# Kernel optimization log

Hardware: AMD Instinct MI355X
Metric: run time of the kernel (lower is better)

The kernel has to match this reference:

```python
import jax, jax.numpy as jnp
import numpy as np

NUM_SLOTS = 7
DIM = 4096
NUM_HEADS = 8
HEAD_DIM = DIM // NUM_HEADS
LN_EPS = 1e-5


def setup_inputs() -> dict:
    key = jax.random.key(0)
    ks = jax.random.split(key, 9)
    B, N = 8, 2048
    x = jax.random.normal(ks[0], (B, N, DIM), dtype=jnp.float32)
    slots = 1e-4 * jax.random.normal(ks[1], (NUM_SLOTS, DIM), dtype=jnp.float32)
    ln_g = jnp.ones((DIM,), jnp.float32)
    ln_b = jnp.zeros((DIM,), jnp.float32)
    # nn.MultiheadAttention packed in-projection: rows [Wq; Wk; Wv], each (DIM, DIM)
    s = 1.0 / np.sqrt(DIM)
    in_proj_w = jax.random.uniform(ks[2], (3 * DIM, DIM), jnp.float32, -s, s)
    in_proj_b = jnp.zeros((3 * DIM,), jnp.float32)
    out_proj_w = jax.random.uniform(ks[3], (DIM, DIM), jnp.float32, -s, s)
    out_proj_b = jnp.zeros((DIM,), jnp.float32)
    alpha = 0.1 * jax.random.normal(ks[4], (1,), jnp.float32)  # nonzero so gate path is active
    return {"x": x, "slots": slots, "ln_g": ln_g, "ln_b": ln_b,
            "in_proj_w": in_proj_w, "in_proj_b": in_proj_b,
            "out_proj_w": out_proj_w, "out_proj_b": out_proj_b, "alpha": alpha}


def _cmrm(x, slots, ln_g, ln_b, in_proj_w, in_proj_b, out_proj_w, out_proj_b, alpha):
    x32 = x.astype(jnp.float32)
    # pre LayerNorm
    mu = jnp.mean(x32, axis=-1, keepdims=True)
    var = jnp.mean(jnp.square(x32 - mu), axis=-1, keepdims=True)
    xn = (x32 - mu) * jax.lax.rsqrt(var + LN_EPS) * ln_g + ln_b  # (B,N,D)
    slots_c = jnp.clip(slots, -10.0, 10.0)  # (Q,D), Q=7
    Wq, Wk, Wv = jnp.split(in_proj_w, 3, axis=0)
    bq, bk, bv = jnp.split(in_proj_b, 3, axis=0)
    q = slots_c @ Wq.T + bq                      # (Q,D), identical for all batches
    k = xn @ Wk.T + bk                           # (B,N,D)
    v = xn @ Wv.T + bv                           # (B,N,D)
    B, N, _ = x.shape
    qh = q.reshape(NUM_SLOTS, NUM_HEADS, HEAD_DIM)          # (Q,H,hd)
    kh = k.reshape(B, N, NUM_HEADS, HEAD_DIM)
    vh = v.reshape(B, N, NUM_HEADS, HEAD_DIM)
    scale = 1.0 / np.sqrt(HEAD_DIM)
    scores = jnp.einsum('qhd,bnhd->bhqn', qh * scale, kh)   # (B,H,Q,N)
    attn = jax.nn.softmax(scores, axis=-1)
    ctx = jnp.einsum('bhqn,bnhd->bqhd', attn, vh).reshape(B, NUM_SLOTS, DIM)
    slots_out = ctx @ out_proj_w.T + out_proj_b             # (B,Q,D)
    slots_res = slots_c[None] + slots_out                   # residual, ungated slots
    gate = jnp.tanh(alpha)                                  # (1,)
    g = jnp.mean(gate * slots_res, axis=1, keepdims=True)   # (B,1,D)
    x_refined = (x32 + g).astype(x.dtype)
    attn_weights = jnp.mean(attn, axis=1)                   # torch avg over heads -> (B,Q,N)
    return x_refined, attn_weights


def reference(x, slots, ln_g, ln_b, in_proj_w, in_proj_b, out_proj_w, out_proj_b, alpha):
    return _cmrm(x, slots, ln_g, ln_b, in_proj_w, in_proj_b, out_proj_w, out_proj_b, alpha)
```

## Files before the change

### kernel.cpp

```cpp
#include <hip/hip_runtime.h>

typedef __attribute__((ext_vector_type(4))) float f32x4;
typedef __attribute__((ext_vector_type(8))) short short8x;
typedef __attribute__((ext_vector_type(4))) unsigned short u16x4;

#define DIM   4096
#define NB    8
#define NN    2048
#define NROWS (NB*NN)
#define NQ    7
#define NHQ   56
#define SCALE 0.04419417382415922f

#define OFF_MU     0L
#define OFF_RSTD   16384L
#define OFF_Q7     32768L
#define OFF_A      61440L
#define OFF_D0     61504L
#define OFF_S1     61568L
#define OFF_SUMEXP 61632L
#define OFF_CTXM   62528L
#define OFF_GFIN   95296L
#define OFF_YM     128064L
#define OFF_UGBF   390208L
#define OFF_SCT    521280L
#define OFF_BIG    1438784L
#define OFF_PART   (OFF_BIG)
#define OFF_XBF    10000000L

__device__ __forceinline__ unsigned short f2bf(float f) {
  union { float f; unsigned int u; } v; v.f = f;
  return (unsigned short)((v.u + 0x7FFFu + ((v.u >> 16) & 1u)) >> 16);
}
__device__ __forceinline__ unsigned short f2bfr(float f) {
  union { float f; unsigned int u; } v; v.f = f;
  return (unsigned short)((v.u + 0x8000u) >> 16);
}
__device__ __forceinline__ float bf2f(unsigned short u) {
  return __uint_as_float((unsigned)u << 16);
}
__device__ __forceinline__ f32x4 ntl4(const float* p) {
  return __builtin_nontemporal_load((const f32x4*)p);
}
__device__ __forceinline__ void nts4(float* p, f32x4 v) {
  __builtin_nontemporal_store(v, (f32x4*)p);
}
__device__ __forceinline__ float waveSum(float v) {
  #pragma unroll
  for (int m = 1; m < 64; m <<= 1) v += __shfl_xor(v, m);
  return v;
}

__global__ __launch_bounds__(256) void k_pre(const float* __restrict__ ipw,
    const float* __restrict__ ipb, const float* __restrict__ slots,
    float* __restrict__ q7, float* __restrict__ ws) {
  const int bid = blockIdx.x, tid = threadIdx.x;
  const int w = tid >> 6, l = tid & 63;
  if (bid == 0) {
    if (tid < 448) (ws + OFF_SUMEXP)[tid] = 0.f;
    else if (tid < 512) (ws + OFF_S1)[tid - 448] = 0.f;
  } else if (bid <= 8) {
    unsigned* u32 = (unsigned*)(ws + OFF_UGBF);
    const long r = 56 + bid - 1;
    #pragma unroll
    for (int j = 0; j < 8; j++) u32[r*2048 + (long)tid*8 + j] = 0u;
  } else if (bid == 9) {
    if (tid < 64) (ws + OFF_A)[tid] = 0.f;
    else if (tid < 128) (ws + OFF_D0)[tid - 64] = 0.f;
  }
  const int d = bid * 4 + w;
  const float* wr = ipw + (long)d * DIM;
  float acc[7] = {0,0,0,0,0,0,0};
  for (int e4 = l; e4 < 1024; e4 += 64) {
    f32x4 wv = ntl4(wr + e4*4);
    #pragma unroll
    for (int s = 0; s < 7; s++) {
      float4 sv = ((const float4*)(slots + (long)s*DIM))[e4];
      sv.x = fminf(fmaxf(sv.x, -10.f), 10.f); sv.y = fminf(fmaxf(sv.y, -10.f), 10.f);
      sv.z = fminf(fmaxf(sv.z, -10.f), 10.f); sv.w = fminf(fmaxf(sv.w, -10.f), 10.f);
      acc[s] += wv.x*sv.x + wv.y*sv.y + wv.z*sv.z + wv.w*sv.w;
    }
  }
  #pragma unroll
  for (int s = 0; s < 7; s++) acc[s] = waveSum(acc[s]);
  if (l == 0) {
    float bq = ipb[d];
    #pragma unroll
    for (int s = 0; s < 7; s++) q7[(long)s*DIM + d] = acc[s] + bq;
  }
}

__global__ __launch_bounds__(256) void k_uproj(const float* __restrict__ ipw,
    const float* __restrict__ ipb, const float* __restrict__ q7,
    float* __restrict__ upart, float* __restrict__ D0arr) {
  __shared__ float qs[7][32];
  const int bid = blockIdx.x, tid = threadIdx.x;
  const int bx = bid & 3, h = (bid >> 2) & 7, c = bid >> 5;
  if (tid < 224) {
    int s = tid >> 5, hd = tid & 31;
    qs[s][hd] = q7[(long)s*DIM + h*512 + c*32 + hd];
  }
  __syncthreads();
  if (bx == 0 && tid < 64) {
    const int l = tid;
    float bk = (l < 32) ? ipb[DIM + h*512 + c*32 + l] : 0.f;
    #pragma unroll
    for (int s = 0; s < 7; s++) {
      float v = (l < 32) ? qs[s][l]*bk : 0.f;
      v = waveSum(v);
      if (l == 0) atomicAdd(&D0arr[h*7 + s], SCALE * v);
    }
  }
  const int e0 = bx*1024 + tid*4;
  float4 acc[7];
  #pragma unroll
  for (int s = 0; s < 7; s++) { acc[s].x = 0; acc[s].y = 0; acc[s].z = 0; acc[s].w = 0; }
  #pragma unroll 4
  for (int hd = 0; hd < 32; hd++) {
    f32x4 wv = ntl4(ipw + ((long)(DIM + h*512 + c*32 + hd))*DIM + e0);
    #pragma unroll
    for (int s = 0; s < 7; s++) {
      float qv = qs[s][hd];
      acc[s].x += qv*wv.x; acc[s].y += qv*wv.y; acc[s].z += qv*wv.z; acc[s].w += qv*wv.w;
    }
  }
  #pragma unroll
  for (int s = 0; s < 7; s++)
    *(float4*)&upart[(long)((c*8 + h)*7 + s)*DIM + e0] = acc[s];
}

__global__ __launch_bounds__(256) void k_ured(const float* __restrict__ upart,
    const float* __restrict__ lng, const float* __restrict__ lnb,
    unsigned short* __restrict__ ugbf, float* __restrict__ Aarr, float* __restrict__ D0arr) {
  const int bid = blockIdx.x, tid = threadIdx.x;
  const int bx = bid & 15, h = bid >> 4;
  const int e = bx*256 + tid, l = tid & 63;
  float ge = lng[e], be = lnb[e];
  #pragma unroll
  for (int s = 0; s < 7; s++) {
    float u = 0;
    #pragma unroll
    for (int c = 0; c < 16; c++) u += upart[(long)((c*8 + h)*7 + s)*DIM + e];
    u *= SCALE;
    ugbf[(long)(h*7 + s)*DIM + e] = f2bf(u * ge);
    float pa = waveSum(u * ge);
    float pd = waveSum(u * be);
    if (l == 0) {
      atomicAdd(&Aarr[h*7 + s], pa);
      atomicAdd(&D0arr[h*7 + s], pd);
    }
  }
}

__global__ __launch_bounds__(256) void k_scores(const float* __restrict__ x,
    const unsigned short* __restrict__ ugbf, const float* __restrict__ Aarr,
    const float* __restrict__ D0arr, float* __restrict__ mu_o, float* __restrict__ rstd_o,
    float* __restrict__ sct, float* __restrict__ sumexp, unsigned short* __restrict__ xbf) {
  __shared__ float xch[3][64][18];
  const int tid = threadIdx.x;
  const int w = tid >> 6, l = tid & 63;
  const int lr = l & 15, lk8 = (l >> 4) * 8;
  const int row0 = blockIdx.x * 16;
  const int b = blockIdx.x >> 7;
  const long arow = (long)(row0 + lr) * DIM;
  unsigned short* xrow = xbf + arow;
  const int kbase = w * 1024;
  f32x4 acc0 = {0,0,0,0}, acc1 = {0,0,0,0}, acc2 = {0,0,0,0}, acc3 = {0,0,0,0};
  float sx = 0.f, sxx = 0.f;
  const long b0 = (long)(0*16 + lr)*DIM, b1 = (long)(1*16 + lr)*DIM,
             b2 = (long)(2*16 + lr)*DIM, b3 = (long)(3*16 + lr)*DIM;
  #pragma unroll 2
  for (int kc = kbase; kc < kbase + 1024; kc += 32) {
    const f32x4 v0 = ntl4(x + arow + kc + lk8);
    const f32x4 v1 = ntl4(x + arow + kc + lk8 + 4);
    sx  += (v0.x + v0.y) + (v0.z + v0.w) + (v1.x + v1.y) + (v1.z + v1.w);
    sxx += v0.x*v0.x + v0.y*v0.y + v0.z*v0.z + v0.w*v0.w
         + v1.x*v1.x + v1.y*v1.y + v1.z*v1.z + v1.w*v1.w;
    short8x a;
    a[0] = (short)f2bfr(v0.x); a[1] = (short)f2bfr(v0.y);
    a[2] = (short)f2bfr(v0.z); a[3] = (short)f2bfr(v0.w);
    a[4] = (short)f2bfr(v1.x); a[5] = (short)f2bfr(v1.y);
    a[6] = (short)f2bfr(v1.z); a[7] = (short)f2bfr(v1.w);
    *(short8x*)(xrow + kc + lk8) = a;
    short8x bb0 = *(const short8x*)(ugbf + b0 + kc + lk8);
    acc0 = __builtin_amdgcn_mfma_f32_16x16x32_bf16(a, bb0, acc0, 0, 0, 0);
    short8x bb1 = *(const short8x*)(ugbf + b1 + kc + lk8);
    acc1 = __builtin_amdgcn_mfma_f32_16x16x32_bf16(a, bb1, acc1, 0, 0, 0);
    short8x bb2 = *(const short8x*)(ugbf + b2 + kc + lk8);
    acc2 = __builtin_amdgcn_mfma_f32_16x16x32_bf16(a, bb2, acc2, 0, 0, 0);
    short8x bb3 = *(const short8x*)(ugbf + b3 + kc + lk8);
    acc3 = __builtin_amdgcn_mfma_f32_16x16x32_bf16(a, bb3, acc3, 0, 0, 0);
  }
  if (w != 0) {
    float* p = xch[w - 1][l];
    #pragma unroll
    for (int i = 0; i < 4; i++) {
      p[i] = acc0[i]; p[4+i] = acc1[i]; p[8+i] = acc2[i]; p[12+i] = acc3[i];
    }
    p[16] = sx; p[17] = sxx;
  }
  __syncthreads();
  if (w != 0) return;
  #pragma unroll
  for (int ww = 0; ww < 3; ww++) {
    const float* p = xch[ww][l];
    #pragma unroll
    for (int i = 0; i < 4; i++) {
      acc0[i] += p[i]; acc1[i] += p[4+i]; acc2[i] += p[8+i]; acc3[i] += p[12+i];
    }
    sx += p[16]; sxx += p[17];
  }
  sx += __shfl_xor(sx, 16);  sx += __shfl_xor(sx, 32);
  sxx += __shfl_xor(sxx, 16); sxx += __shfl_xor(sxx, 32);
  float muv = sx * (1.0f/DIM);
  float var = sxx * (1.0f/DIM) - muv*muv;
  float rsv = rsqrtf(var + 1e-5f);
  if (l < 16) { mu_o[row0 + l] = muv; rstd_o[row0 + l] = rsv; }
  float es0 = 0, es1 = 0, es2 = 0, es3 = 0;
  #pragma unroll
  for (int i = 0; i < 4; i++) {
    const int rl = (l >> 4)*4 + i;
    const float mur_ = __shfl(muv, rl);
    const float rs_  = __shfl(rsv, rl);
    {
      int hq = 0*16 + lr; float Ah = Aarr[hq], Dh = D0arr[hq];
      float e = __expf(rs_*(acc0[i] - mur_*Ah) + Dh);
      sct[(long)hq*NROWS + row0 + rl] = e; es0 += e;
    }
    {
      int hq = 1*16 + lr; float Ah = Aarr[hq], Dh = D0arr[hq];
      float e = __expf(rs_*(acc1[i] - mur_*Ah) + Dh);
      sct[(long)hq*NROWS + row0 + rl] = e; es1 += e;
    }
    {
      int hq = 2*16 + lr; float Ah = Aarr[hq], Dh = D0arr[hq];
      float e = __expf(rs_*(acc2[i] - mur_*Ah) + Dh);
      sct[(long)hq*NROWS + row0 + rl] = e; es2 += e;
    }
    if (lr < 8) {
      int hq = 3*16 + lr; float Ah = Aarr[hq], Dh = D0arr[hq];
      float e = __expf(rs_*(acc3[i] - mur_*Ah) + Dh);
      sct[(long)hq*NROWS + row0 + rl] = e; es3 += e;
    }
  }
  es0 += __shfl_xor(es0, 16); es0 += __shfl_xor(es0, 32);
  es1 += __shfl_xor(es1, 16); es1 += __shfl_xor(es1, 32);
  es2 += __shfl_xor(es2, 16); es2 += __shfl_xor(es2, 32);
  es3 += __shfl_xor(es3, 16); es3 += __shfl_xor(es3, 32);
  if (l < 16) {
    atomicAdd(&sumexp[b*NHQ + 0*16 + l], es0);
    atomicAdd(&sumexp[b*NHQ + 1*16 + l], es1);
    atomicAdd(&sumexp[b*NHQ + 2*16 + l], es2);
    if (l < 8) atomicAdd(&sumexp[b*NHQ + 3*16 + l], es3);
  }
}

__global__ __launch_bounds__(256) void k_ypart(const unsigned short* __restrict__ xbf,
    const float* __restrict__ sct, const float* __restrict__ sumexp,
    const float* __restrict__ mu, const float* __restrict__ rstd,
    float* __restrict__ part, float* __restrict__ s1, float* __restrict__ out_attn) {
  __shared__ float rinv[56];
  __shared__ float amr[8][128];
  __shared__ float psm[56][128];
  const int bid = blockIdx.x, tid = threadIdx.x;
  const int b = bid >> 6, ec = (bid >> 4) & 3, nc = bid & 15;
  const int row0 = b*NN + nc*128;
  if (tid < 56) rinv[tid] = 1.0f / sumexp[b*NHQ + tid];
  __syncthreads();
  for (int i = tid; i < 1024; i += 256) {
    const int h = i >> 7, nn = i & 127, row = row0 + nn;
    float amv = 0;
    #pragma unroll
    for (int q = 0; q < 7; q++) {
      float p = sct[(long)(h*7 + q)*NROWS + row] * rinv[h*7 + q];
      amv += p;
      psm[h*7 + q][nn] = p;
    }
    amv *= (1.0f/7.0f);
    amr[h][nn] = amv * rstd[row];
  }
  __syncthreads();
  if (ec == 0) {
    for (int i = tid; i < 896; i += 256) {
      const int q = i / 128, nn = i % 128;
      float s = 0;
      #pragma unroll
      for (int h = 0; h < 8; h++) s += psm[h*7 + q][nn];
      out_attn[((long)(b*NQ + q))*NN + nc*128 + nn] = s * 0.125f;
    }
    {
      const int h = tid >> 5, sl = tid & 31;
      float v = 0;
      #pragma unroll
      for (int nn = sl; nn < 128; nn += 32) v += amr[h][nn] * mu[row0 + nn];
      #pragma unroll
      for (int m = 1; m < 32; m <<= 1) v += __shfl_xor(v, m);
      if (sl == 0) atomicAdd(&s1[b*8 + h], v);
    }
  }
  const int e = ec*1024 + tid*4;
  float ax[8], ay[8], az[8], aw[8];
  #pragma unroll
  for (int h = 0; h < 8; h++) { ax[h]=0; ay[h]=0; az[h]=0; aw[h]=0; }
  const unsigned short* xp = xbf + (long)row0*DIM + e;
  #pragma unroll 2
  for (int nn = 0; nn < 128; nn++) {
    const u16x4 xv = *(const u16x4*)(xp + (long)nn*DIM);
    const float xx = bf2f(xv.x), xy = bf2f(xv.y), xz = bf2f(xv.z), xw = bf2f(xv.w);
    #pragma unroll
    for (int h = 0; h < 8; h++) {
      float a = amr[h][nn];
      ax[h] += a*xx; ay[h] += a*xy; az[h] += a*xz; aw[h] += a*xw;
    }
  }
  #pragma unroll
  for (int h = 0; h < 8; h++) {
    float4 o; o.x = ax[h]; o.y = ay[h]; o.z = az[h]; o.w = aw[h];
    *(float4*)&part[((long)(nc*64 + b*8 + h))*DIM + e] = o;
  }
}

__global__ __launch_bounds__(256) void k_yred(const float* __restrict__ part,
    const float* __restrict__ s1, const float* __restrict__ lng, const float* __restrict__ lnb,
    float* __restrict__ ym) {
  const long i4 = (long)blockIdx.x*256 + threadIdx.x;
  const float4* p4 = (const float4*)part;
  float4 s = p4[i4];
  #pragma unroll
  for (int nc = 1; nc < 16; nc++) {
    float4 v = p4[(long)nc*65536 + i4];
    s.x += v.x; s.y += v.y; s.z += v.z; s.w += v.w;
  }
  const int bh = (int)(i4 >> 10), e4 = (int)(i4 & 1023);
  float sv = s1[bh];
  float4 g = ((const float4*)lng)[e4], bb = ((const float4*)lnb)[e4];
  float4 o;
  o.x = g.x*(s.x - sv) + bb.x; o.y = g.y*(s.y - sv) + bb.y;
  o.z = g.z*(s.z - sv) + bb.z; o.w = g.w*(s.w - sv) + bb.w;
  ((float4*)ym)[i4] = o;
}

__global__ __launch_bounds__(256) void k_ctxm(const float* __restrict__ ipw,
    const float* __restrict__ ipb, const float* __restrict__ ym, float* __restrict__ ctxm) {
  const int w = threadIdx.x >> 6, l = threadIdx.x & 63;
  const int d = blockIdx.x*4 + w;
  const int h = d >> 9;
  const float* wr = ipw + ((long)(2*DIM + d))*DIM;
  float acc[8] = {0,0,0,0,0,0,0,0};
  for (int e4 = l; e4 < 1024; e4 += 64) {
    f32x4 wv = ntl4(wr + e4*4);
    #pragma unroll
    for (int b = 0; b < 8; b++) {
      float4 y = ((const float4*)(ym + (long)(b*8 + h)*DIM))[e4];
      acc[b] += wv.x*y.x + wv.y*y.y + wv.z*y.z + wv.w*y.w;
    }
  }
  #pragma unroll
  for (int b = 0; b < 8; b++) acc[b] = waveSum(acc[b]);
  if (l == 0) {
    float bias = ipb[2*DIM + d];
    #pragma unroll
    for (int b = 0; b < 8; b++) ctxm[(long)b*DIM + d] = acc[b] + bias;
  }
}

__global__ __launch_bounds__(256) void k_gvec(const float* __restrict__ opw,
    const float* __restrict__ opb, const float* __restrict__ ctxm, const float* __restrict__ slots,
    const float* __restrict__ alpha, float* __restrict__ gfin) {
  const int w = threadIdx.x >> 6, l = threadIdx.x & 63;
  const int d = blockIdx.x*4 + w;
  const float* wr = opw + (long)d*DIM;
  float acc[8] = {0,0,0,0,0,0,0,0};
  for (int e4 = l; e4 < 1024; e4 += 64) {
    f32x4 wv = ntl4(wr + e4*4);
    #pragma unroll
    for (int b = 0; b < 8; b++) {
      float4 c = ((const float4*)(ctxm + (long)b*DIM))[e4];
      acc[b] += wv.x*c.x + wv.y*c.y + wv.z*c.z + wv.w*c.w;
    }
  }
  #pragma unroll
  for (int b = 0; b < 8; b++) acc[b] = waveSum(acc[b]);
  if (l == 0) {
    float smv = 0;
    #pragma unroll
    for (int q = 0; q < 7; q++)
      smv += fminf(fmaxf(slots[(long)q*DIM + d], -10.f), 10.f);
    smv *= (1.0f/7.0f);
    float t = tanhf(alpha[0]);
    float base = smv + opb[d];
    #pragma unroll
    for (int b = 0; b < 8; b++) gfin[(long)b*DIM + d] = t * (base + acc[b]);
  }
}

__global__ __launch_bounds__(256) void k_refine(const unsigned short* __restrict__ xbf,
    const float* __restrict__ gfin, float* __restrict__ out) {
  const float4* g4 = (const float4*)gfin;
  const long total = (long)NROWS * 1024;
  for (long i4 = (long)blockIdx.x*256 + threadIdx.x; i4 < total; i4 += (long)gridDim.x*256) {
    const long b = i4 >> 21;
    const int e4 = (int)(i4 & 1023);
    const u16x4 xv = *(const u16x4*)(xbf + i4*4);
    const float4 gv = g4[b*1024 + e4];
    f32x4 o;
    o.x = bf2f(xv.x) + gv.x; o.y = bf2f(xv.y) + gv.y;
    o.z = bf2f(xv.z) + gv.z; o.w = bf2f(xv.w) + gv.w;
    nts4(out + i4*4, o);
  }
}

extern "C" void kernel_launch(void* const* d_in, const int* in_sizes, int n_in,
                              void* d_out, int out_size, void* d_ws, size_t ws_size,
                              hipStream_t stream) {
  const float* x     = (const float*)d_in[0];
  const float* slots = (const float*)d_in[1];
  const float* lng   = (const float*)d_in[2];
  const float* lnb   = (const float*)d_in[3];
  const float* ipw   = (const float*)d_in[4];
  const float* ipb   = (const float*)d_in[5];
  const float* opw   = (const float*)d_in[6];
  const float* opb   = (const float*)d_in[7];
  const float* alpha = (const float*)d_in[8];
  float* out = (float*)d_out;
  float* ws  = (float*)d_ws;

  float* mu     = ws + OFF_MU;
  float* rstd   = ws + OFF_RSTD;
  float* q7     = ws + OFF_Q7;
  float* Aarr   = ws + OFF_A;
  float* D0arr  = ws + OFF_D0;
  float* s1     = ws + OFF_S1;
  float* sumexp = ws + OFF_SUMEXP;
  float* ctxm   = ws + OFF_CTXM;
  float* gfin   = ws + OFF_GFIN;
  float* ym     = ws + OFF_YM;
  unsigned short* ugbf = (unsigned short*)(ws + OFF_UGBF);
  float* sct    = ws + OFF_SCT;
  float* upart  = ws + OFF_BIG;
  float* part   = ws + OFF_PART;
  unsigned short* xbf = (unsigned short*)(ws + OFF_XBF);
  float* out_attn = out + (long)NROWS * DIM;

  hipLaunchKernelGGL(k_pre,    dim3(1024), dim3(256), 0, stream, ipw, ipb, slots, q7, ws);
  hipLaunchKernelGGL(k_uproj,  dim3(512),  dim3(256), 0, stream, ipw, ipb, q7, upart, D0arr);
  hipLaunchKernelGGL(k_ured,   dim3(128),  dim3(256), 0, stream, upart, lng, lnb, ugbf, Aarr, D0arr);
  hipLaunchKernelGGL(k_scores, dim3(1024), dim3(256), 0, stream, x, ugbf, Aarr, D0arr, mu, rstd, sct, sumexp, xbf);
  hipLaunchKernelGGL(k_ypart,  dim3(512),  dim3(256), 0, stream, xbf, sct, sumexp, mu, rstd, part, s1, out_attn);
  hipLaunchKernelGGL(k_yred,   dim3(256),  dim3(256), 0, stream, part, s1, lng, lnb, ym);
  hipLaunchKernelGGL(k_ctxm,   dim3(1024), dim3(256), 0, stream, ipw, ipb, ym, ctxm);
  hipLaunchKernelGGL(k_gvec,   dim3(1024), dim3(256), 0, stream, opw, opb, ctxm, slots, alpha, gfin);
  hipLaunchKernelGGL(k_refine, dim3(8192), dim3(256), 0, stream, xbf, gfin, out);
}
```

Baseline: 368.9 us.

## Stage x rows through LDS with coalesced loads in scores kernel

The scores kernel now loads x with coalesced row-major float4 accesses, where 16 threads cover each row, instead of the strided per-lane MFMA fragment pattern. It converts to bf16 into an LDS tile, then reads MFMA A-fragments from LDS in 512-column stages, with each wave handling a 128-column slice per stage. Row statistics are reduced with shuffles within each row group and shared through LDS. This is meant to improve global load coalescing and bf16 store efficiency, at the cost of two block barriers per stage and extra LDS traffic.

```diff
diff --git a/kernel.cpp b/kernel.cpp
--- a/kernel.cpp
+++ b/kernel.cpp
@@ -156,48 +156,61 @@
     const unsigned short* __restrict__ ugbf, const float* __restrict__ Aarr,
     const float* __restrict__ D0arr, float* __restrict__ mu_o, float* __restrict__ rstd_o,
     float* __restrict__ sct, float* __restrict__ sumexp, unsigned short* __restrict__ xbf) {
-  __shared__ float xch[3][64][18];
+  __shared__ __align__(16) unsigned short xs[16][520];
+  __shared__ float xch[3][64][16];
+  __shared__ float sred[16][2];
   const int tid = threadIdx.x;
   const int w = tid >> 6, l = tid & 63;
   const int lr = l & 15, lk8 = (l >> 4) * 8;
   const int row0 = blockIdx.x * 16;
   const int b = blockIdx.x >> 7;
-  const long arow = (long)(row0 + lr) * DIM;
-  unsigned short* xrow = xbf + arow;
-  const int kbase = w * 1024;
+  const int r = tid >> 4, c = tid & 15;
+  const long xrow = (long)(row0 + r) * DIM;
   f32x4 acc0 = {0,0,0,0}, acc1 = {0,0,0,0}, acc2 = {0,0,0,0}, acc3 = {0,0,0,0};
   float sx = 0.f, sxx = 0.f;
   const long b0 = (long)(0*16 + lr)*DIM, b1 = (long)(1*16 + lr)*DIM,
              b2 = (long)(2*16 + lr)*DIM, b3 = (long)(3*16 + lr)*DIM;
-  #pragma unroll 2
-  for (int kc = kbase; kc < kbase + 1024; kc += 32) {
-    const f32x4 v0 = ntl4(x + arow + kc + lk8);
-    const f32x4 v1 = ntl4(x + arow + kc + lk8 + 4);
-    sx  += (v0.x + v0.y) + (v0.z + v0.w) + (v1.x + v1.y) + (v1.z + v1.w);
-    sxx += v0.x*v0.x + v0.y*v0.y + v0.z*v0.z + v0.w*v0.w
-         + v1.x*v1.x + v1.y*v1.y + v1.z*v1.z + v1.w*v1.w;
-    short8x a;
-    a[0] = (short)f2bfr(v0.x); a[1] = (short)f2bfr(v0.y);
-    a[2] = (short)f2bfr(v0.z); a[3] = (short)f2bfr(v0.w);
-    a[4] = (short)f2bfr(v1.x); a[5] = (short)f2bfr(v1.y);
-    a[6] = (short)f2bfr(v1.z); a[7] = (short)f2bfr(v1.w);
-    *(short8x*)(xrow + kc + lk8) = a;
-    short8x bb0 = *(const short8x*)(ugbf + b0 + kc + lk8);
-    acc0 = __builtin_amdgcn_mfma_f32_16x16x32_bf16(a, bb0, acc0, 0, 0, 0);
-    short8x bb1 = *(const short8x*)(ugbf + b1 + kc + lk8);
-    acc1 = __builtin_amdgcn_mfma_f32_16x16x32_bf16(a, bb1, acc1, 0, 0, 0);
-    short8x bb2 = *(const short8x*)(ugbf + b2 + kc + lk8);
-    acc2 = __builtin_amdgcn_mfma_f32_16x16x32_bf16(a, bb2, acc2, 0, 0, 0);
-    short8x bb3 = *(const short8x*)(ugbf + b3 + kc + lk8);
-    acc3 = __builtin_amdgcn_mfma_f32_16x16x32_bf16(a, bb3, acc3, 0, 0, 0);
-  }
+  for (int s = 0; s < 8; s++) {
+    const int kc0 = s * 512;
+    f32x4 v[8];
+    #pragma unroll
+    for (int j = 0; j < 8; j++)
+      v[j] = ntl4(x + xrow + kc0 + j*64 + c*4);
+    #pragma unroll
+    for (int j = 0; j < 8; j++) {
+      sx  += (v[j].x + v[j].y) + (v[j].z + v[j].w);
+      sxx += v[j].x*v[j].x + v[j].y*v[j].y + v[j].z*v[j].z + v[j].w*v[j].w;
+      u16x4 a;
+      a.x = f2bfr(v[j].x); a.y = f2bfr(v[j].y);
+      a.z = f2bfr(v[j].z); a.w = f2bfr(v[j].w);
+      *(u16x4*)&xs[r][j*64 + c*4] = a;
+      *(u16x4*)(xbf + xrow + kc0 + j*64 + c*4) = a;
+    }
+    __syncthreads();
+    const long kw = kc0 + w*128;
+    #pragma unroll
+    for (int kk = 0; kk < 128; kk += 32) {
+      short8x a = *(const short8x*)&xs[lr][w*128 + kk + lk8];
+      short8x bb0 = *(const short8x*)(ugbf + b0 + kw + kk + lk8);
+      acc0 = __builtin_amdgcn_mfma_f32_16x16x32_bf16(a, bb0, acc0, 0, 0, 0);
+      short8x bb1 = *(const short8x*)(ugbf + b1 + kw + kk + lk8);
+      acc1 = __builtin_amdgcn_mfma_f32_16x16x32_bf16(a, bb1, acc1, 0, 0, 0);
+      short8x bb2 = *(const short8x*)(ugbf + b2 + kw + kk + lk8);
+      acc2 = __builtin_amdgcn_mfma_f32_16x16x32_bf16(a, bb2, acc2, 0, 0, 0);
+      short8x bb3 = *(const short8x*)(ugbf + b3 + kw + kk + lk8);
+      acc3 = __builtin_amdgcn_mfma_f32_16x16x32_bf16(a, bb3, acc3, 0, 0, 0);
+    }
+    __syncthreads();
+  }
+  #pragma unroll
+  for (int m = 1; m <= 8; m <<= 1) { sx += __shfl_xor(sx, m); sxx += __shfl_xor(sxx, m); }
+  if (c == 0) { sred[r][0] = sx; sred[r][1] = sxx; }
   if (w != 0) {
     float* p = xch[w - 1][l];
     #pragma unroll
     for (int i = 0; i < 4; i++) {
       p[i] = acc0[i]; p[4+i] = acc1[i]; p[8+i] = acc2[i]; p[12+i] = acc3[i];
     }
-    p[16] = sx; p[17] = sxx;
   }
   __syncthreads();
   if (w != 0) return;
@@ -208,12 +221,9 @@
     for (int i = 0; i < 4; i++) {
       acc0[i] += p[i]; acc1[i] += p[4+i]; acc2[i] += p[8+i]; acc3[i] += p[12+i];
     }
-    sx += p[16]; sxx += p[17];
-  }
-  sx += __shfl_xor(sx, 16);  sx += __shfl_xor(sx, 32);
-  sxx += __shfl_xor(sxx, 16); sxx += __shfl_xor(sxx, 32);
-  float muv = sx * (1.0f/DIM);
-  float var = sxx * (1.0f/DIM) - muv*muv;
+  }
+  float muv = sred[lr][0] * (1.0f/DIM);
+  float var = sred[lr][1] * (1.0f/DIM) - muv*muv;
   float rsv = rsqrtf(var + 1e-5f);
   if (l < 16) { mu_o[row0 + l] = muv; rstd_o[row0 + l] = rsv; }
   float es0 = 0, es1 = 0, es2 = 0, es3 = 0;
```

Measured after the change: 348.1 us, median of 3. 1.06x faster.
